# Optimization experiments

Hardware: AMD Instinct MI355X
Metric: run time of the kernel (lower is better)

## Reference

```python
import jax, jax.numpy as jnp
import numpy as np

N_NODES = 100000
N_EDGES = 1600000
IN_CH, HID_CH, OUT_CH = 128, 128, 64


def glorot(key, fan_in, fan_out):
    lim = np.sqrt(6.0 / (fan_in + fan_out)).astype(np.float32)
    return jax.random.uniform(key, (fan_in, fan_out), jnp.float32, -lim, lim)


def gcn_conv(x, src, dst, W, b):
    """PyG GCNConv: add self-loops, symmetric deg^-1/2 normalization,
    linear transform, scatter-add aggregation at targets, plus bias."""
    n = x.shape[0]
    xw = x @ W  # [N, F_out]
    loop = jnp.arange(n)
    s = jnp.concatenate([src, loop])  # sources (message origin)
    d = jnp.concatenate([dst, loop])  # targets (aggregation site)
    deg = jax.ops.segment_sum(jnp.ones_like(d, dtype=xw.dtype), d, num_segments=n)
    dinv = jnp.where(deg > 0, jax.lax.rsqrt(deg), 0.0)
    norm = dinv[s] * dinv[d]  # [E+N]
    out = jax.ops.segment_sum(norm[:, None] * xw[s], d, num_segments=n)
    return out + b


def setup_inputs() -> dict:
    key = jax.random.key(0)
    ks = jax.random.split(key, 8)
    x = jax.random.normal(ks[0], (N_NODES, IN_CH), jnp.float32)
    edge_index = jax.random.randint(ks[1], (2, N_EDGES), 0, N_NODES, jnp.int64)
    return {
        "x": x,
        "edge_index": edge_index,
        "W1": glorot(ks[2], IN_CH, HID_CH),
        "b1": jnp.zeros((HID_CH,), jnp.float32),
        "W2": glorot(ks[3], HID_CH, HID_CH),
        "b2": jnp.zeros((HID_CH,), jnp.float32),
        "W3": glorot(ks[4], HID_CH, OUT_CH),
        "b3": jnp.zeros((OUT_CH,), jnp.float32),
    }


def reference(x, edge_index, W1, b1, W2, b2, W3, b3):
    src, dst = edge_index[0], edge_index[1]
    # eval mode: dropout is identity
    h = jax.nn.relu(gcn_conv(x, src, dst, W1, b1))
    h = jax.nn.relu(gcn_conv(h, src, dst, W2, b2))
    h = gcn_conv(h, src, dst, W3, b3)
    return jax.nn.log_softmax(h, axis=1)
```

## Files before the change

kernel.cpp:

```cpp
#include <hip/hip_runtime.h>
#include <math.h>


#define NN 100000
#define NE 1600000
#define NBUK 391
#define BCAP 4608

typedef float floatx4 __attribute__((ext_vector_type(4)));
typedef short short8 __attribute__((ext_vector_type(8)));

__device__ __forceinline__ unsigned short f2bf(float f) {
    unsigned u = __float_as_uint(f);
    unsigned r = (u + 0x7fffu + ((u >> 16) & 1u)) >> 16;
    return (unsigned short)r;
}
__device__ __forceinline__ float bflo(unsigned u) { return __uint_as_float(u << 16); }
__device__ __forceinline__ float bfhi(unsigned u) { return __uint_as_float(u & 0xffff0000u); }

__global__ __launch_bounds__(256) void k_wprep(const float* __restrict__ W, unsigned short* __restrict__ Wtg,
                                               int K, int NC) {
    int idx = blockIdx.x * 256 + threadIdx.x;
    if (idx >= NC * K) return;
    int n = idx / K, k = idx - n * K;
    Wtg[idx] = f2bf(W[k * NC + n]);
}

__global__ __launch_bounds__(256) void k_bucket(const int4* __restrict__ src4, const int4* __restrict__ dst4,
                                                int* __restrict__ bcur, int* __restrict__ bbuf, int E) {
    __shared__ int hist[NBUK];
    __shared__ int base[NBUK];
    int t = threadIdx.x;
    for (int b = t; b < NBUK; b += 256) hist[b] = 0;
    __syncthreads();
    int E4 = E >> 2;
    int q0 = blockIdx.x * 1024;
    #pragma unroll
    for (int j = 0; j < 4; j++) {
        int q = q0 + j * 256 + t;
        if (q < E4) {
            int4 d = dst4[q];
            atomicAdd(&hist[d.x >> 8], 1);
            atomicAdd(&hist[d.y >> 8], 1);
            atomicAdd(&hist[d.z >> 8], 1);
            atomicAdd(&hist[d.w >> 8], 1);
        }
    }
    __syncthreads();
    for (int b = t; b < NBUK; b += 256) {
        int c = hist[b];
        base[b] = c ? atomicAdd(&bcur[b], c) : 0;
        hist[b] = 0;
    }
    __syncthreads();
    #pragma unroll
    for (int j = 0; j < 4; j++) {
        int q = q0 + j * 256 + t;
        if (q < E4) {
            int4 s = src4[q];
            int4 d = dst4[q];
            int sv[4] = {s.x, s.y, s.z, s.w};
            int dv[4] = {d.x, d.y, d.z, d.w};
            #pragma unroll
            for (int u = 0; u < 4; u++) {
                int b = dv[u] >> 8;
                int r = atomicAdd(&hist[b], 1);
                int pos = base[b] + r;
                if (pos < BCAP) bbuf[b * BCAP + pos] = (sv[u] << 8) | (dv[u] & 255);
            }
        }
    }
}

__global__ void k_scanbuckets(const int* __restrict__ bcur, int* __restrict__ bbase, int nb,
                              int* __restrict__ row_ptr, int n, int E) {
    int lane = threadIdx.x;
    int carry = 0;
    for (int base = 0; base < nb; base += 64) {
        int idx = base + lane;
        int v = (idx < nb) ? min(bcur[idx], BCAP) : 0;
        int orig = v;
        #pragma unroll
        for (int o = 1; o < 64; o <<= 1) {
            int u = __shfl_up(v, o);
            if (lane >= o) v += u;
        }
        if (idx < nb) bbase[idx] = carry + v - orig;
        carry += __shfl(v, 63);
    }
    if (lane == 0) row_ptr[n] = E;
}

__global__ __launch_bounds__(256) void k_build(const int* __restrict__ bcur, const int* __restrict__ bbase,
                                               const int* __restrict__ bbuf,
                                               int* __restrict__ row_ptr, int* __restrict__ csr, int N) {
    __shared__ int sh[256];
    __shared__ int cur[256];
    __shared__ int loc[BCAP];
    int b = blockIdx.x, t = threadIdx.x;
    int cnt = min(bcur[b], BCAP);
    int gbase = bbase[b];
    const int* bp = bbuf + b * BCAP;
    sh[t] = 0;
    __syncthreads();
    for (int i = t; i < cnt; i += 256) atomicAdd(&sh[bp[i] & 255], 1);
    __syncthreads();
    int v = sh[t];
    for (int o = 1; o < 256; o <<= 1) {
        int u = (t >= o) ? sh[t - o] : 0;
        __syncthreads();
        sh[t] += u;
        __syncthreads();
    }
    int excl = sh[t] - v;
    int node = b * 256 + t;
    if (node < N) row_ptr[node] = gbase + excl;
    cur[t] = excl;
    __syncthreads();
    for (int i = t; i < cnt; i += 256) {
        int p = bp[i];
        int r = atomicAdd(&cur[p & 255], 1);
        loc[r] = p >> 8;
    }
    __syncthreads();
    for (int i = t; i < cnt; i += 256) csr[gbase + i] = loc[i];
}

__global__ __launch_bounds__(256) void k_dinv(const int* __restrict__ row_ptr, float* __restrict__ dinv, int n) {
    int i = blockIdx.x * 256 + threadIdx.x;
    if (i < n) {
        int d = row_ptr[i + 1] - row_ptr[i];
        dinv[i] = rsqrtf((float)d + 1.0f);
    }
}


template <int NC, bool CVT>
__global__ __launch_bounds__(256) void k_mfma(const void* __restrict__ Av, const unsigned short* __restrict__ Wtg,
                                              const float* __restrict__ dinv, unsigned short* __restrict__ Y, int M) {
    constexpr int K = 128;
    constexpr int NT = NC / 16;
    constexpr int NU = NC / 32;
    __shared__ unsigned short Wt[NC][136];
    __shared__ unsigned short Ost[4][16][NC + 8];
    int t = threadIdx.x;
    constexpr int NV = NC * K / 8;
    for (int idx = t; idx < NV; idx += 256) {
        int nrow = idx >> 4;
        int chunk = idx & 15;
        *(uint4*)&Wt[nrow][chunk * 8] = *(const uint4*)(Wtg + nrow * K + chunk * 8);
    }
    __syncthreads();
    int lane = t & 63, wid = t >> 6;
    int col = lane & 15, quad = lane >> 4;
    int nstrips = M / 16;
    int stride = gridDim.x * 4;
    int s = blockIdx.x * 4 + wid;
    if (s >= nstrips) return;

    auto loadA = [&](int strip, short8 af[4]) {
        int row0 = strip * 16;
        if (CVT) {
            const float* Af = (const float*)Av + (size_t)(row0 + col) * K + quad * 8;
            #pragma unroll
            for (int ks = 0; ks < 4; ks++) {
                float4 f0 = *(const float4*)(Af + ks * 32);
                float4 f1 = *(const float4*)(Af + ks * 32 + 4);
                short8 v;
                v[0] = (short)f2bf(f0.x); v[1] = (short)f2bf(f0.y); v[2] = (short)f2bf(f0.z); v[3] = (short)f2bf(f0.w);
                v[4] = (short)f2bf(f1.x); v[5] = (short)f2bf(f1.y); v[6] = (short)f2bf(f1.z); v[7] = (short)f2bf(f1.w);
                af[ks] = v;
            }
        } else {
            const unsigned short* Ab = (const unsigned short*)Av + (size_t)(row0 + col) * K + quad * 8;
            #pragma unroll
            for (int ks = 0; ks < 4; ks++) af[ks] = *(const short8*)(Ab + ks * 32);
        }
    };

    short8 cur[4];
    loadA(s, cur);
    while (true) {
        int snext = s + stride;
        bool has = (snext < nstrips);
        short8 nxt[4];
        if (has) loadA(snext, nxt);

        floatx4 acc[NT];
        #pragma unroll
        for (int i = 0; i < NT; i++) acc[i] = (floatx4){0.f, 0.f, 0.f, 0.f};
        #pragma unroll
        for (int ks = 0; ks < 4; ks++) {
            #pragma unroll
            for (int nt = 0; nt < NT; nt++) {
                short8 bfrag = *(const short8*)&Wt[nt * 16 + col][ks * 32 + quad * 8];
                acc[nt] = __builtin_amdgcn_mfma_f32_16x16x32_bf16(cur[ks], bfrag, acc[nt], 0, 0, 0);
            }
        }
        int row0 = s * 16;
        #pragma unroll
        for (int r = 0; r < 4; r++) {
            int row = row0 + quad * 4 + r;
            float dv = dinv[row];
            #pragma unroll
            for (int nt = 0; nt < NT; nt++) {
                Ost[wid][quad * 4 + r][nt * 16 + col] = f2bf(acc[nt][r] * dv);
            }
        }
        #pragma unroll
        for (int i = 0; i < NU; i++) {
            int idx = i * 64 + lane;
            int rr = idx >> 4, cc = idx & 15;
            int rr2 = (NC == 128) ? (idx >> 4) : (idx >> 3);
            int cc2 = (NC == 128) ? (idx & 15) : (idx & 7);
            (void)rr; (void)cc;
            ((uint4*)&Y[(size_t)(row0 + rr2) * NC])[cc2] = *(uint4*)&Ost[wid][rr2][cc2 * 8];
        }
        if (!has) break;
        s = snext;
        #pragma unroll
        for (int ks = 0; ks < 4; ks++) cur[ks] = nxt[ks];
    }
}


__device__ __forceinline__ void acc8(float* a, uint4 v) {
    a[0] += bflo(v.x); a[1] += bfhi(v.x);
    a[2] += bflo(v.y); a[3] += bfhi(v.y);
    a[4] += bflo(v.z); a[5] += bfhi(v.z);
    a[6] += bflo(v.w); a[7] += bfhi(v.w);
}

__global__ __launch_bounds__(256) void k_gather_relu_bf(const uint4* __restrict__ y, const int* __restrict__ csr,
                                                        const int* __restrict__ row_ptr, const float* __restrict__ dinv,
                                                        const float* __restrict__ bias, uint4* __restrict__ h, int n) {
    int node = blockIdx.x * 16 + (threadIdx.x >> 4);
    int c = threadIdx.x & 15;
    if (node >= n) return;
    int s0 = row_ptr[node], s1 = row_ptr[node + 1];
    float a[8] = {};
    acc8(a, y[(size_t)node * 16 + c]);
    int p = s0;
    for (; p + 4 <= s1; p += 4) {
        int i0 = csr[p], i1 = csr[p + 1], i2 = csr[p + 2], i3 = csr[p + 3];
        uint4 v0 = y[(size_t)i0 * 16 + c];
        uint4 v1 = y[(size_t)i1 * 16 + c];
        uint4 v2 = y[(size_t)i2 * 16 + c];
        uint4 v3 = y[(size_t)i3 * 16 + c];
        acc8(a, v0); acc8(a, v1); acc8(a, v2); acc8(a, v3);
    }
    for (; p < s1; p++) acc8(a, y[(size_t)csr[p] * 16 + c]);
    float s = dinv[node];
    float4 b0 = ((const float4*)bias)[c * 2];
    float4 b1 = ((const float4*)bias)[c * 2 + 1];
    float r0 = fmaxf(s * a[0] + b0.x, 0.f), r1 = fmaxf(s * a[1] + b0.y, 0.f);
    float r2 = fmaxf(s * a[2] + b0.z, 0.f), r3 = fmaxf(s * a[3] + b0.w, 0.f);
    float r4 = fmaxf(s * a[4] + b1.x, 0.f), r5 = fmaxf(s * a[5] + b1.y, 0.f);
    float r6 = fmaxf(s * a[6] + b1.z, 0.f), r7 = fmaxf(s * a[7] + b1.w, 0.f);
    uint4 o;
    o.x = ((unsigned)f2bf(r1) << 16) | f2bf(r0);
    o.y = ((unsigned)f2bf(r3) << 16) | f2bf(r2);
    o.z = ((unsigned)f2bf(r5) << 16) | f2bf(r4);
    o.w = ((unsigned)f2bf(r7) << 16) | f2bf(r6);
    h[(size_t)node * 16 + c] = o;
}

__global__ __launch_bounds__(256) void k_gather_lsm_bf(const uint4* __restrict__ y, const int* __restrict__ csr,
                                                       const int* __restrict__ row_ptr, const float* __restrict__ dinv,
                                                       const float* __restrict__ bias, float4* __restrict__ out4, int n) {
    int node = blockIdx.x * 32 + (threadIdx.x >> 3);
    int c = threadIdx.x & 7;
    if (node >= n) return;
    int s0 = row_ptr[node], s1 = row_ptr[node + 1];
    float a[8] = {};
    acc8(a, y[(size_t)node * 8 + c]);
    int p = s0;
    for (; p + 4 <= s1; p += 4) {
        int i0 = csr[p], i1 = csr[p + 1], i2 = csr[p + 2], i3 = csr[p + 3];
        uint4 v0 = y[(size_t)i0 * 8 + c];
        uint4 v1 = y[(size_t)i1 * 8 + c];
        uint4 v2 = y[(size_t)i2 * 8 + c];
        uint4 v3 = y[(size_t)i3 * 8 + c];
        acc8(a, v0); acc8(a, v1); acc8(a, v2); acc8(a, v3);
    }
    for (; p < s1; p++) acc8(a, y[(size_t)csr[p] * 8 + c]);
    float s = dinv[node];
    float4 b0 = ((const float4*)bias)[c * 2];
    float4 b1 = ((const float4*)bias)[c * 2 + 1];
    float v[8];
    v[0] = s * a[0] + b0.x; v[1] = s * a[1] + b0.y; v[2] = s * a[2] + b0.z; v[3] = s * a[3] + b0.w;
    v[4] = s * a[4] + b1.x; v[5] = s * a[5] + b1.y; v[6] = s * a[6] + b1.z; v[7] = s * a[7] + b1.w;
    float m = v[0];
    #pragma unroll
    for (int i = 1; i < 8; i++) m = fmaxf(m, v[i]);
    #pragma unroll
    for (int o = 4; o > 0; o >>= 1) m = fmaxf(m, __shfl_xor(m, o));
    float sum = 0.f;
    #pragma unroll
    for (int i = 0; i < 8; i++) sum += expf(v[i] - m);
    #pragma unroll
    for (int o = 4; o > 0; o >>= 1) sum += __shfl_xor(sum, o);
    float lse = m + logf(sum);
    out4[(size_t)node * 16 + c * 2]     = make_float4(v[0] - lse, v[1] - lse, v[2] - lse, v[3] - lse);
    out4[(size_t)node * 16 + c * 2 + 1] = make_float4(v[4] - lse, v[5] - lse, v[6] - lse, v[7] - lse);
}


extern "C" void kernel_launch(void* const* d_in, const int* in_sizes, int n_in,
                              void* d_out, int out_size, void* d_ws, size_t ws_size,
                              hipStream_t stream) {
    const float* x  = (const float*)d_in[0];
    const int*   ei = (const int*)d_in[1];
    const float* W1 = (const float*)d_in[2];
    const float* b1 = (const float*)d_in[3];
    const float* W2 = (const float*)d_in[4];
    const float* b2 = (const float*)d_in[5];
    const float* W3 = (const float*)d_in[6];
    const float* b3 = (const float*)d_in[7];
    float* out = (float*)d_out;

    const int N = NN, E = NE;
    const int nb = (N + 255) / 256;

    char* ws = (char*)d_ws;
    size_t off = 0;
    auto alloc = [&](size_t bytes) -> void* {
        void* p = ws + off;
        off += bytes;
        off = (off + 255) & ~(size_t)255;
        return p;
    };
    int*            row_ptr = (int*)alloc((size_t)(N + 1) * 4);
    float*          dinvv   = (float*)alloc((size_t)N * 4);
    int*            bcur    = (int*)alloc(512 * 4);
    int*            bbase   = (int*)alloc(512 * 4);
    int*            bbuf    = (int*)alloc((size_t)NBUK * BCAP * 4);
    int*            csr     = (int*)alloc((size_t)E * 4);
    unsigned short* wt1     = (unsigned short*)alloc(128 * 128 * 2);
    unsigned short* wt2     = (unsigned short*)alloc(128 * 128 * 2);
    unsigned short* wt3     = (unsigned short*)alloc(64 * 128 * 2);
    unsigned short* yb      = (unsigned short*)alloc((size_t)N * 128 * 2);
    unsigned short* hb      = (unsigned short*)alloc((size_t)N * 128 * 2);
    (void)ws_size; (void)in_sizes; (void)n_in; (void)out_size;

    const int* srcp = ei;
    const int* dstp = ei + E;

    hipMemsetAsync(bcur, 0, 512 * 4, stream);
    k_wprep<<<64, 256, 0, stream>>>(W1, wt1, 128, 128);
    k_wprep<<<64, 256, 0, stream>>>(W2, wt2, 128, 128);
    k_wprep<<<32, 256, 0, stream>>>(W3, wt3, 128, 64);
    k_bucket<<<(E + 4095) / 4096, 256, 0, stream>>>((const int4*)srcp, (const int4*)dstp, bcur, bbuf, E);
    k_scanbuckets<<<1, 64, 0, stream>>>(bcur, bbase, NBUK, row_ptr, N, E);
    k_build<<<NBUK, 256, 0, stream>>>(bcur, bbase, bbuf, row_ptr, csr, N);
    k_dinv<<<nb, 256, 0, stream>>>(row_ptr, dinvv, N);

    k_mfma<128, true><<<512, 256, 0, stream>>>(x, wt1, dinvv, yb, N);
    k_gather_relu_bf<<<N / 16, 256, 0, stream>>>((const uint4*)yb, csr, row_ptr, dinvv, b1, (uint4*)hb, N);
    k_mfma<128, false><<<512, 256, 0, stream>>>(hb, wt2, dinvv, yb, N);
    k_gather_relu_bf<<<N / 16, 256, 0, stream>>>((const uint4*)yb, csr, row_ptr, dinvv, b2, (uint4*)hb, N);
    k_mfma<64, false><<<512, 256, 0, stream>>>(hb, wt3, dinvv, yb, N);
    k_gather_lsm_bf<<<N / 32, 256, 0, stream>>>((const uint4*)yb, csr, row_ptr, dinvv, b3, (float4*)out, N);
}
```

Baseline: 336.1 us.

## Merge weight-prep launches, fold dinv into CSR build, enlarge MFMA grids

Replaces the three weight-transpose launches with one combined kernel and computes dinv inside k_build from the per-node counts, which removes the separate k_dinv launch. k_bucket now keeps the src/dst loads in registers from the histogram pass so the edge arrays are not read twice. The MFMA grids grow from 512 to 768 blocks to spread the strips over more waves. Together these cut launch count and redundant global reads, at the cost of more registers in k_bucket.

```diff
diff --git a/kernel.cpp b/kernel.cpp
--- a/kernel.cpp
+++ b/kernel.cpp
@@ -18,12 +18,23 @@
 __device__ __forceinline__ float bflo(unsigned u) { return __uint_as_float(u << 16); }
 __device__ __forceinline__ float bfhi(unsigned u) { return __uint_as_float(u & 0xffff0000u); }
 
-__global__ __launch_bounds__(256) void k_wprep(const float* __restrict__ W, unsigned short* __restrict__ Wtg,
-                                               int K, int NC) {
+__global__ __launch_bounds__(256) void k_wprep_all(const float* __restrict__ W1, const float* __restrict__ W2,
+                                                   const float* __restrict__ W3,
+                                                   unsigned short* __restrict__ wt1, unsigned short* __restrict__ wt2,
+                                                   unsigned short* __restrict__ wt3) {
     int idx = blockIdx.x * 256 + threadIdx.x;
-    if (idx >= NC * K) return;
-    int n = idx / K, k = idx - n * K;
-    Wtg[idx] = f2bf(W[k * NC + n]);
+    if (idx < 16384) {
+        int n = idx >> 7, k = idx & 127;
+        wt1[idx] = f2bf(W1[k * 128 + n]);
+    } else if (idx < 32768) {
+        int i = idx - 16384;
+        int n = i >> 7, k = i & 127;
+        wt2[i] = f2bf(W2[k * 128 + n]);
+    } else if (idx < 40960) {
+        int i = idx - 32768;
+        int n = i >> 7, k = i & 127;
+        wt3[i] = f2bf(W3[k * 64 + n]);
+    }
 }
 
 __global__ __launch_bounds__(256) void k_bucket(const int4* __restrict__ src4, const int4* __restrict__ dst4,
@@ -35,15 +46,19 @@
     __syncthreads();
     int E4 = E >> 2;
     int q0 = blockIdx.x * 1024;
+    int4 sv[4], dv[4];
+    bool valid[4];
     #pragma unroll
     for (int j = 0; j < 4; j++) {
         int q = q0 + j * 256 + t;
-        if (q < E4) {
-            int4 d = dst4[q];
-            atomicAdd(&hist[d.x >> 8], 1);
-            atomicAdd(&hist[d.y >> 8], 1);
-            atomicAdd(&hist[d.z >> 8], 1);
-            atomicAdd(&hist[d.w >> 8], 1);
+        valid[j] = (q < E4);
+        if (valid[j]) {
+            sv[j] = src4[q];
+            dv[j] = dst4[q];
+            atomicAdd(&hist[dv[j].x >> 8], 1);
+            atomicAdd(&hist[dv[j].y >> 8], 1);
+            atomicAdd(&hist[dv[j].z >> 8], 1);
+            atomicAdd(&hist[dv[j].w >> 8], 1);
         }
     }
     __syncthreads();
@@ -55,18 +70,15 @@
     __syncthreads();
     #pragma unroll
     for (int j = 0; j < 4; j++) {
-        int q = q0 + j * 256 + t;
-        if (q < E4) {
-            int4 s = src4[q];
-            int4 d = dst4[q];
-            int sv[4] = {s.x, s.y, s.z, s.w};
-            int dv[4] = {d.x, d.y, d.z, d.w};
+        if (valid[j]) {
+            int ss[4] = {sv[j].x, sv[j].y, sv[j].z, sv[j].w};
+            int dd[4] = {dv[j].x, dv[j].y, dv[j].z, dv[j].w};
             #pragma unroll
             for (int u = 0; u < 4; u++) {
-                int b = dv[u] >> 8;
+                int b = dd[u] >> 8;
                 int r = atomicAdd(&hist[b], 1);
                 int pos = base[b] + r;
-                if (pos < BCAP) bbuf[b * BCAP + pos] = (sv[u] << 8) | (dv[u] & 255);
+                if (pos < BCAP) bbuf[b * BCAP + pos] = (ss[u] << 8) | (dd[u] & 255);
             }
         }
     }
@@ -93,7 +105,8 @@
 
 __global__ __launch_bounds__(256) void k_build(const int* __restrict__ bcur, const int* __restrict__ bbase,
                                                const int* __restrict__ bbuf,
-                                               int* __restrict__ row_ptr, int* __restrict__ csr, int N) {
+                                               int* __restrict__ row_ptr, int* __restrict__ csr,
+                                               float* __restrict__ dinv, int N) {
     __shared__ int sh[256];
     __shared__ int cur[256];
     __shared__ int loc[BCAP];
@@ -114,7 +127,10 @@
     }
     int excl = sh[t] - v;
     int node = b * 256 + t;
-    if (node < N) row_ptr[node] = gbase + excl;
+    if (node < N) {
+        row_ptr[node] = gbase + excl;
+        dinv[node] = rsqrtf((float)v + 1.0f);
+    }
     cur[t] = excl;
     __syncthreads();
     for (int i = t; i < cnt; i += 256) {
@@ -124,14 +140,6 @@
     }
     __syncthreads();
     for (int i = t; i < cnt; i += 256) csr[gbase + i] = loc[i];
-}
-
-__global__ __launch_bounds__(256) void k_dinv(const int* __restrict__ row_ptr, float* __restrict__ dinv, int n) {
-    int i = blockIdx.x * 256 + threadIdx.x;
-    if (i < n) {
-        int d = row_ptr[i + 1] - row_ptr[i];
-        dinv[i] = rsqrtf((float)d + 1.0f);
-    }
 }
 
 
@@ -144,10 +152,8 @@
     __shared__ unsigned short Wt[NC][136];
     __shared__ unsigned short Ost[4][16][NC + 8];
     int t = threadIdx.x;
-    constexpr int NV = NC * K / 8;
-    for (int idx = t; idx < NV; idx += 256) {
-        int nrow = idx >> 4;
-        int chunk = idx & 15;
+    for (int idx = t; idx < NC * 16; idx += 256) {
+        int nrow = idx >> 4, chunk = idx & 15;
         *(uint4*)&Wt[nrow][chunk * 8] = *(const uint4*)(Wtg + nrow * K + chunk * 8);
     }
     __syncthreads();
@@ -200,21 +206,17 @@
         int row0 = s * 16;
         #pragma unroll
         for (int r = 0; r < 4; r++) {
-            int row = row0 + quad * 4 + r;
-            float dv = dinv[row];
-            #pragma unroll
-            for (int nt = 0; nt < NT; nt++) {
+            float dv = dinv[row0 + quad * 4 + r];
+            #pragma unroll
+            for (int nt = 0; nt < NT; nt++)
                 Ost[wid][quad * 4 + r][nt * 16 + col] = f2bf(acc[nt][r] * dv);
-            }
         }
         #pragma unroll
         for (int i = 0; i < NU; i++) {
             int idx = i * 64 + lane;
-            int rr = idx >> 4, cc = idx & 15;
-            int rr2 = (NC == 128) ? (idx >> 4) : (idx >> 3);
-            int cc2 = (NC == 128) ? (idx & 15) : (idx & 7);
-            (void)rr; (void)cc;
-            ((uint4*)&Y[(size_t)(row0 + rr2) * NC])[cc2] = *(uint4*)&Ost[wid][rr2][cc2 * 8];
+            int rr = (NC == 128) ? (idx >> 4) : (idx >> 3);
+            int cc = (NC == 128) ? (idx & 15) : (idx & 7);
+            ((uint4*)&Y[(size_t)(row0 + rr) * NC])[cc] = *(uint4*)&Ost[wid][rr][cc * 8];
         }
         if (!has) break;
         s = snext;
@@ -320,7 +322,6 @@
     float* out = (float*)d_out;
 
     const int N = NN, E = NE;
-    const int nb = (N + 255) / 256;
 
     char* ws = (char*)d_ws;
     size_t off = 0;
@@ -347,18 +348,15 @@
     const int* dstp = ei + E;
 
     hipMemsetAsync(bcur, 0, 512 * 4, stream);
-    k_wprep<<<64, 256, 0, stream>>>(W1, wt1, 128, 128);
-    k_wprep<<<64, 256, 0, stream>>>(W2, wt2, 128, 128);
-    k_wprep<<<32, 256, 0, stream>>>(W3, wt3, 128, 64);
+    k_wprep_all<<<160, 256, 0, stream>>>(W1, W2, W3, wt1, wt2, wt3);
     k_bucket<<<(E + 4095) / 4096, 256, 0, stream>>>((const int4*)srcp, (const int4*)dstp, bcur, bbuf, E);
     k_scanbuckets<<<1, 64, 0, stream>>>(bcur, bbase, NBUK, row_ptr, N, E);
-    k_build<<<NBUK, 256, 0, stream>>>(bcur, bbase, bbuf, row_ptr, csr, N);
-    k_dinv<<<nb, 256, 0, stream>>>(row_ptr, dinvv, N);
-
-    k_mfma<128, true><<<512, 256, 0, stream>>>(x, wt1, dinvv, yb, N);
+    k_build<<<NBUK, 256, 0, stream>>>(bcur, bbase, bbuf, row_ptr, csr, dinvv, N);
+
+    k_mfma<128, true><<<768, 256, 0, stream>>>(x, wt1, dinvv, yb, N);
     k_gather_relu_bf<<<N / 16, 256, 0, stream>>>((const uint4*)yb, csr, row_ptr, dinvv, b1, (uint4*)hb, N);
-    k_mfma<128, false><<<512, 256, 0, stream>>>(hb, wt2, dinvv, yb, N);
+    k_mfma<128, false><<<768, 256, 0, stream>>>(hb, wt2, dinvv, yb, N);
     k_gather_relu_bf<<<N / 16, 256, 0, stream>>>((const uint4*)yb, csr, row_ptr, dinvv, b2, (uint4*)hb, N);
-    k_mfma<64, false><<<512, 256, 0, stream>>>(hb, wt3, dinvv, yb, N);
+    k_mfma<64, false><<<768, 256, 0, stream>>>(hb, wt3, dinvv, yb, N);
     k_gather_lsm_bf<<<N / 32, 256, 0, stream>>>((const uint4*)yb, csr, row_ptr, dinvv, b3, (float4*)out, N);
 }
```

After: 331.5 us. No clear change (-1.4%).
